# Kernel optimization log

Hardware: AMD Instinct MI355X
Metric: run time of the kernel (lower is better)

Reference implementation:

```python
import jax, jax.numpy as jnp
import numpy as np

N_NODES = 50000
N_EDGES = 640000
DIM_IN = 128
DIM_OUT = 32
NUM_GRAPHS = 64


def setup_inputs() -> dict:
    key = jax.random.key(0)
    ks = jax.random.split(key, 8)
    x = jax.random.normal(ks[0], (N_NODES, DIM_IN), dtype=jnp.float32)
    edge_index = jax.random.randint(ks[1], (2, N_EDGES), 0, N_NODES, dtype=jnp.int64)
    batch = jnp.sort(jax.random.randint(ks[2], (N_NODES,), 0, NUM_GRAPHS, dtype=jnp.int64))
    s = 1.0 / np.sqrt(DIM_IN)
    W1 = jax.random.normal(ks[3], (DIM_IN, DIM_IN), dtype=jnp.float32) * s
    b1 = jnp.zeros((DIM_IN,), dtype=jnp.float32)
    W2 = jax.random.normal(ks[4], (DIM_IN, DIM_IN), dtype=jnp.float32) * s
    b2 = jnp.zeros((DIM_IN,), dtype=jnp.float32)
    Wh = jax.random.normal(ks[5], (DIM_IN, DIM_OUT), dtype=jnp.float32) * s
    bh = jnp.zeros((DIM_OUT,), dtype=jnp.float32)
    return {"x": x, "edge_index": edge_index, "batch": batch,
            "W1": W1, "b1": b1, "W2": W2, "b2": b2, "Wh": Wh, "bh": bh}


def _gcn_conv(x, src, dst, norm, W, b):
    # GCNConv: h = x @ W; out[i] = sum_{(j->i)} norm_e * h[j] + b
    h = x @ W
    msg = h[src] * norm[:, None]                      # [E+N, D] gather + scale
    out = jax.ops.segment_sum(msg, dst, num_segments=x.shape[0])
    return out + b


def reference(x, edge_index, batch, W1, b1, W2, b2, Wh, bh):
    n = x.shape[0]
    loops = jnp.arange(n, dtype=edge_index.dtype)
    src = jnp.concatenate([edge_index[0], loops])     # add self-loops
    dst = jnp.concatenate([edge_index[1], loops])
    # symmetric normalization: deg^{-1/2}[src] * deg^{-1/2}[dst]
    deg = jax.ops.segment_sum(jnp.ones_like(dst, dtype=x.dtype), dst, num_segments=n)
    dinv = jnp.where(deg > 0, jax.lax.rsqrt(deg), 0.0)
    norm = dinv[src] * dinv[dst]

    h = jax.nn.relu(_gcn_conv(x, src, dst, norm, W1, b1))   # dropout = identity (eval)
    h = jax.nn.relu(_gcn_conv(h, src, dst, norm, W2, b2))
    pooled = jax.ops.segment_sum(h, batch, num_segments=NUM_GRAPHS)  # global_add_pool
    logits = pooled @ Wh + bh
    return jax.nn.log_softmax(logits, axis=1)
```

## Files before the change

kernel.cpp:

```cpp
#include <hip/hip_runtime.h>
#include <hip/hip_bf16.h>
#include <math.h>

#define N_NODES 50000
#define N_EDGES 640000
#define DIM     128
#define NGRAPH  64
#define DOUT    32
#define CAP     64
#define LDSS 136
#define LDSF 132

#define G_GEMM  782
#define B_W2    (G_GEMM)
#define N_W2    64
#define B_ZERO  (B_W2 + N_W2)
#define N_ZERO  32
#define B_FILL  (B_ZERO + N_ZERO)
#define N_FILL  2500
#define G_FRONT (B_FILL + N_FILL)

typedef unsigned short u16;
typedef __attribute__((ext_vector_type(8))) short bf16x8;
typedef __attribute__((ext_vector_type(4))) float f32x4;

__device__ __forceinline__ u16 f2bf(float f) {
    unsigned u = __float_as_uint(f);
    return (u16)((u + 0x7FFFu + ((u >> 16) & 1u)) >> 16);
}
__device__ __forceinline__ float bf2f(u16 h) {
    return __uint_as_float(((unsigned)h) << 16);
}
__device__ __forceinline__ short2 cvt2(float x, float y) {
    __hip_bfloat162 h = __float22bfloat162_rn(make_float2(x, y));
    return *(short2*)&h;
}
__device__ __forceinline__ void upk(unsigned u, float& lo, float& hi) {
    lo = __uint_as_float(u << 16);
    hi = __uint_as_float(u & 0xFFFF0000u);
}

__global__ __launch_bounds__(256) void k_front(const float* __restrict__ X,
                                               const int* __restrict__ src,
                                               const int* __restrict__ dst,
                                               int* __restrict__ cnt,
                                               int* __restrict__ bucket,
                                               const float* __restrict__ W1,
                                               const float* __restrict__ W2,
                                               u16* __restrict__ W2s,
                                               float* __restrict__ pooled,
                                               u16* __restrict__ Y) {
    __shared__ u16 Wl[16384];
    int b   = blockIdx.x;
    int tid = threadIdx.x;

    if (b < G_GEMM) {
        const float4* W14 = (const float4*)W1;
#pragma unroll
        for (int i = 0; i < 16; ++i) {
            int q = i * 256 + tid;
            float4 vv = W14[q];
            int base = q * 4;
            int k = base >> 7, n0 = base & 127;
            int rb = ((n0 >> 4) * 4 + (k >> 5)) * 512 + ((k & 31) >> 3) * 128
                   + (k & 7) + (n0 & 15) * 8;
            Wl[rb]      = f2bf(vv.x);
            Wl[rb + 8]  = f2bf(vv.y);
            Wl[rb + 16] = f2bf(vv.z);
            Wl[rb + 24] = f2bf(vv.w);
        }
        int wv   = tid >> 6;
        int lane = tid & 63;
        int row0 = b * 64 + wv * 16;
        int m    = lane & 15;
        int quad = lane >> 4;
        int ar = min(row0 + m, N_NODES - 1);
        const float* Arow = X + (size_t)ar * DIM;
        bf16x8 a[4];
#pragma unroll
        for (int kc = 0; kc < 4; ++kc) {
            const float4* p4 = (const float4*)(Arow + kc * 32 + quad * 8);
            float4 p = p4[0], q = p4[1];
            short2 s0 = cvt2(p.x, p.y), s1 = cvt2(p.z, p.w);
            short2 s2 = cvt2(q.x, q.y), s3 = cvt2(q.z, q.w);
            bf16x8 av;
            av[0] = s0.x; av[1] = s0.y; av[2] = s1.x; av[3] = s1.y;
            av[4] = s2.x; av[5] = s2.y; av[6] = s3.x; av[7] = s3.y;
            a[kc] = av;
        }
        __syncthreads();
#pragma unroll
        for (int nt = 0; nt < 8; ++nt) {
            f32x4 acc = {0.f, 0.f, 0.f, 0.f};
#pragma unroll
            for (int kc = 0; kc < 4; ++kc) {
                bf16x8 bb = *(const bf16x8*)(&Wl[((nt * 4 + kc) * 64 + lane) * 8]);
                acc = __builtin_amdgcn_mfma_f32_16x16x32_bf16(a[kc], bb, acc, 0, 0, 0);
            }
            int col = nt * 16 + m;
#pragma unroll
            for (int r = 0; r < 4; ++r) {
                int rr = row0 + quad * 4 + r;
                if (rr < N_NODES) Y[(size_t)rr * DIM + col] = f2bf(acc[r]);
            }
        }
    } else if (b < B_ZERO) {
        int t = (b - B_W2) * 256 + tid;
        int j = t & 7, lane = (t >> 3) & 63, kc = (t >> 9) & 3, nt = t >> 11;
        int k = kc * 32 + (lane >> 4) * 8 + j;
        int n = nt * 16 + (lane & 15);
        W2s[t] = f2bf(W2[k * 128 + n]);
    } else if (b < B_FILL) {
        int t = (b - B_ZERO) * 256 + tid;
        pooled[t] = 0.f;
    } else {
        int e = (b - B_FILL) * 256 + tid;
        int d = dst[e];
        int s = src[e];
        int pos = atomicAdd(&cnt[d], 1);
        bucket[d * CAP + pos] = s;
    }
}

__global__ __launch_bounds__(256) void k_agg_gemm(const u16* __restrict__ H,
                                                  const int* __restrict__ bucket,
                                                  const int* __restrict__ cnt,
                                                  const float* __restrict__ bias,
                                                  const u16* __restrict__ Ws,
                                                  u16* __restrict__ Y) {
    __shared__ u16 As[16][LDSS];
    int tid    = threadIdx.x;
    int nloc   = tid >> 4;
    int lane16 = tid & 15;
    int node   = blockIdx.x * 16 + nloc;

    int deg = cnt[node];
    float dself = rsqrtf((float)(deg + 1));
    int e0 = node * CAP, e1 = e0 + deg;
    const uint4* H4 = (const uint4*)H;
    uint4 sv = H4[(size_t)node * 16 + lane16];
    float a0[8], a1[8] = {}, a2[8] = {}, a3[8] = {};
    {
        float lo, hi;
        upk(sv.x, lo, hi); a0[0] = dself * lo; a0[1] = dself * hi;
        upk(sv.y, lo, hi); a0[2] = dself * lo; a0[3] = dself * hi;
        upk(sv.z, lo, hi); a0[4] = dself * lo; a0[5] = dself * hi;
        upk(sv.w, lo, hi); a0[6] = dself * lo; a0[7] = dself * hi;
    }
    for (int e = e0; e < e1; e += 8) {
        int4 c0 = *(const int4*)(bucket + e);
        int4 c1 = *(const int4*)(bucket + e + 4);
        int   idx[8];
        float w[8];
        uint4 v[8];
        int   cd[8];
        idx[0] = c0.x; idx[1] = c0.y; idx[2] = c0.z; idx[3] = c0.w;
        idx[4] = c1.x; idx[5] = c1.y; idx[6] = c1.z; idx[7] = c1.w;
#pragma unroll
        for (int u = 0; u < 8; ++u) {
            bool in = (e + u) < e1;
            w[u]   = in ? 1.f : 0.f;
            idx[u] = in ? idx[u] : 0;
        }
#pragma unroll
        for (int u = 0; u < 8; ++u) cd[u] = cnt[idx[u]];
#pragma unroll
        for (int u = 0; u < 8; ++u) v[u] = H4[(size_t)idx[u] * 16 + lane16];
#pragma unroll
        for (int u = 0; u < 8; ++u) w[u] *= rsqrtf((float)(cd[u] + 1));
#pragma unroll
        for (int u = 0; u < 8; ++u) {
            float* a = (u & 3) == 0 ? a0 : (u & 3) == 1 ? a1 : (u & 3) == 2 ? a2 : a3;
            float lo, hi;
            upk(v[u].x, lo, hi); a[0] = fmaf(w[u], lo, a[0]); a[1] = fmaf(w[u], hi, a[1]);
            upk(v[u].y, lo, hi); a[2] = fmaf(w[u], lo, a[2]); a[3] = fmaf(w[u], hi, a[3]);
            upk(v[u].z, lo, hi); a[4] = fmaf(w[u], lo, a[4]); a[5] = fmaf(w[u], hi, a[5]);
            upk(v[u].w, lo, hi); a[6] = fmaf(w[u], lo, a[6]); a[7] = fmaf(w[u], hi, a[7]);
        }
    }
    {
        float di = dself;
        const float4* b4 = (const float4*)bias;
        float4 blo = b4[lane16 * 2], bhi = b4[lane16 * 2 + 1];
        float r0 = fmaxf(di * (a0[0] + a1[0] + a2[0] + a3[0]) + blo.x, 0.f);
        float r1 = fmaxf(di * (a0[1] + a1[1] + a2[1] + a3[1]) + blo.y, 0.f);
        float r2 = fmaxf(di * (a0[2] + a1[2] + a2[2] + a3[2]) + blo.z, 0.f);
        float r3 = fmaxf(di * (a0[3] + a1[3] + a2[3] + a3[3]) + blo.w, 0.f);
        float r4 = fmaxf(di * (a0[4] + a1[4] + a2[4] + a3[4]) + bhi.x, 0.f);
        float r5 = fmaxf(di * (a0[5] + a1[5] + a2[5] + a3[5]) + bhi.y, 0.f);
        float r6 = fmaxf(di * (a0[6] + a1[6] + a2[6] + a3[6]) + bhi.z, 0.f);
        float r7 = fmaxf(di * (a0[7] + a1[7] + a2[7] + a3[7]) + bhi.w, 0.f);
        short2 s0 = cvt2(r0, r1), s1 = cvt2(r2, r3), s2 = cvt2(r4, r5), s3 = cvt2(r6, r7);
        uint4 o;
        o.x = *(unsigned*)&s0; o.y = *(unsigned*)&s1;
        o.z = *(unsigned*)&s2; o.w = *(unsigned*)&s3;
        *(uint4*)(&As[nloc][lane16 * 8]) = o;
    }
    __syncthreads();

    int wv   = tid >> 6;
    int lane = tid & 63;
    int m    = lane & 15;
    int quad = lane >> 4;
    bf16x8 a[4];
#pragma unroll
    for (int kc = 0; kc < 4; ++kc)
        a[kc] = *(const bf16x8*)(&As[m][kc * 32 + quad * 8]);
    float di[4];
#pragma unroll
    for (int r = 0; r < 4; ++r)
        di[r] = rsqrtf((float)(cnt[blockIdx.x * 16 + quad * 4 + r] + 1));
#pragma unroll
    for (int i = 0; i < 2; ++i) {
        int nt = wv * 2 + i;
        f32x4 acc = {0.f, 0.f, 0.f, 0.f};
#pragma unroll
        for (int kc = 0; kc < 4; ++kc) {
            bf16x8 b = *(const bf16x8*)(Ws + ((size_t)(nt * 4 + kc) * 64 + lane) * 8);
            acc = __builtin_amdgcn_mfma_f32_16x16x32_bf16(a[kc], b, acc, 0, 0, 0);
        }
        int col = nt * 16 + m;
#pragma unroll
        for (int r = 0; r < 4; ++r) {
            int rr = blockIdx.x * 16 + quad * 4 + r;
            Y[(size_t)rr * DIM + col] = f2bf(acc[r] * di[r]);
        }
    }
}

__global__ __launch_bounds__(256) void k_agg_pool(const u16* __restrict__ H,
                                                  const int* __restrict__ bucket,
                                                  const int* __restrict__ cnt,
                                                  const float* __restrict__ bias,
                                                  const int* __restrict__ batch,
                                                  float* __restrict__ pooled) {
    __shared__ float As[16][LDSF];
    __shared__ int bs[16];
    int tid  = threadIdx.x;
    int nloc = tid >> 4;
    int lane = tid & 15;
    int node = blockIdx.x * 16 + nloc;

    int deg = cnt[node];
    int e0 = node * CAP, e1 = e0 + deg;
    const uint4* H4 = (const uint4*)H;
    uint4 sv = H4[(size_t)node * 16 + lane];
    float a0[8], a1[8] = {}, a2[8] = {}, a3[8] = {};
    upk(sv.x, a0[0], a0[1]); upk(sv.y, a0[2], a0[3]);
    upk(sv.z, a0[4], a0[5]); upk(sv.w, a0[6], a0[7]);
    for (int e = e0; e < e1; e += 8) {
        int4 c0 = *(const int4*)(bucket + e);
        int4 c1 = *(const int4*)(bucket + e + 4);
        int   idx[8];
        float w[8];
        uint4 v[8];
        idx[0] = c0.x; idx[1] = c0.y; idx[2] = c0.z; idx[3] = c0.w;
        idx[4] = c1.x; idx[5] = c1.y; idx[6] = c1.z; idx[7] = c1.w;
#pragma unroll
        for (int u = 0; u < 8; ++u) {
            bool in = (e + u) < e1;
            w[u]   = in ? 1.f : 0.f;
            idx[u] = in ? idx[u] : 0;
        }
#pragma unroll
        for (int u = 0; u < 8; ++u) v[u] = H4[(size_t)idx[u] * 16 + lane];
#pragma unroll
        for (int u = 0; u < 8; ++u) {
            float* a = (u & 3) == 0 ? a0 : (u & 3) == 1 ? a1 : (u & 3) == 2 ? a2 : a3;
            float lo, hi;
            upk(v[u].x, lo, hi); a[0] = fmaf(w[u], lo, a[0]); a[1] = fmaf(w[u], hi, a[1]);
            upk(v[u].y, lo, hi); a[2] = fmaf(w[u], lo, a[2]); a[3] = fmaf(w[u], hi, a[3]);
            upk(v[u].z, lo, hi); a[4] = fmaf(w[u], lo, a[4]); a[5] = fmaf(w[u], hi, a[5]);
            upk(v[u].w, lo, hi); a[6] = fmaf(w[u], lo, a[6]); a[7] = fmaf(w[u], hi, a[7]);
        }
    }
    {
        float di = rsqrtf((float)(deg + 1));
        const float4* b4 = (const float4*)bias;
        float4 blo = b4[lane * 2], bhi = b4[lane * 2 + 1];
        float4 olo, ohi;
        olo.x = fmaxf(di * (a0[0] + a1[0] + a2[0] + a3[0]) + blo.x, 0.f);
        olo.y = fmaxf(di * (a0[1] + a1[1] + a2[1] + a3[1]) + blo.y, 0.f);
        olo.z = fmaxf(di * (a0[2] + a1[2] + a2[2] + a3[2]) + blo.z, 0.f);
        olo.w = fmaxf(di * (a0[3] + a1[3] + a2[3] + a3[3]) + blo.w, 0.f);
        ohi.x = fmaxf(di * (a0[4] + a1[4] + a2[4] + a3[4]) + bhi.x, 0.f);
        ohi.y = fmaxf(di * (a0[5] + a1[5] + a2[5] + a3[5]) + bhi.y, 0.f);
        ohi.z = fmaxf(di * (a0[6] + a1[6] + a2[6] + a3[6]) + bhi.z, 0.f);
        ohi.w = fmaxf(di * (a0[7] + a1[7] + a2[7] + a3[7]) + bhi.w, 0.f);
        *(float4*)(&As[nloc][lane * 8])     = olo;
        *(float4*)(&As[nloc][lane * 8 + 4]) = ohi;
    }
    if (lane == 0) bs[nloc] = batch[node];
    __syncthreads();

    if (tid < 128) {
        float acc = 0.f;
        int cb = bs[0];
#pragma unroll
        for (int n = 0; n < 16; ++n) {
            int b = bs[n];
            if (b != cb) {
                atomicAdd(&pooled[cb * DIM + tid], acc);
                acc = 0.f; cb = b;
            }
            acc += As[n][tid];
        }
        atomicAdd(&pooled[cb * DIM + tid], acc);
    }
}

__global__ __launch_bounds__(64) void k_head(const float* __restrict__ pooled,
                                             const float* __restrict__ Wh,
                                             const float* __restrict__ bh,
                                             float* __restrict__ out) {
    int g = blockIdx.x;
    int lane = threadIdx.x;
    int c = lane & 31;
    const float* p = pooled + g * DIM;
    float lg = bh[c];
#pragma unroll 8
    for (int k = 0; k < DIM; ++k) lg = fmaf(p[k], Wh[k * DOUT + c], lg);
    float m = lg;
    for (int off = 16; off >= 1; off >>= 1) m = fmaxf(m, __shfl_xor(m, off, 32));
    float ex = expf(lg - m);
    float s = ex;
    for (int off = 16; off >= 1; off >>= 1) s += __shfl_xor(s, off, 32);
    if (lane < 32) out[g * DOUT + c] = lg - m - logf(s);
}

extern "C" void kernel_launch(void* const* d_in, const int* in_sizes, int n_in,
                              void* d_out, int out_size, void* d_ws, size_t ws_size,
                              hipStream_t stream) {
    const float* x     = (const float*)d_in[0];
    const int*   ei    = (const int*)d_in[1];
    const int*   batch = (const int*)d_in[2];
    const float* W1    = (const float*)d_in[3];
    const float* b1    = (const float*)d_in[4];
    const float* W2    = (const float*)d_in[5];
    const float* b2    = (const float*)d_in[6];
    const float* Wh    = (const float*)d_in[7];
    const float* bh    = (const float*)d_in[8];
    float* out = (float*)d_out;
    const int* src = ei;
    const int* dst = ei + N_EDGES;

    char* ws = (char*)d_ws;
    size_t off = 0;
    auto alloc = [&](size_t bytes) {
        void* p = ws + off;
        off += (bytes + 255) & ~(size_t)255;
        return p;
    };
    u16*   bufA   = (u16*) alloc((size_t)N_NODES * DIM * 2);
    u16*   bufB   = (u16*) alloc((size_t)N_NODES * DIM * 2);
    int*   cnt    = (int*) alloc((size_t)N_NODES * 4);
    int*   bucket = (int*) alloc((size_t)N_NODES * CAP * 4);
    u16*   W2s    = (u16*) alloc((size_t)DIM * DIM * 2);
    float* pooled = (float*)alloc((size_t)NGRAPH * DIM * 4);
    (void)ws_size; (void)in_sizes; (void)n_in; (void)out_size;

    hipMemsetAsync(cnt, 0, (size_t)N_NODES * 4, stream);

    k_front   <<<G_FRONT, 256, 0, stream>>>(x, src, dst, cnt, bucket, W1, W2,
                                            W2s, pooled, bufA);
    k_agg_gemm<<<N_NODES / 16, 256, 0, stream>>>(bufA, bucket, cnt, b1, W2s, bufB);
    k_agg_pool<<<N_NODES / 16, 256, 0, stream>>>(bufB, bucket, cnt, b2, batch, pooled);

    k_head<<<NGRAPH, 64, 0, stream>>>(pooled, Wh, bh, out);
}
```

Before: 197.0 us.

## Pre-swizzle W1 in a prep kernel and prefetch bucket indices in aggregation

Moves the bf16 conversion and swizzle of W1 (plus the W2 swizzle and the pooled zeroing) into a small separate prep kernel. The GEMM blocks in k_front now read pre-swizzled W1 fragments straight from global memory instead of each of the 782 blocks rebuilding a 32KB LDS copy and waiting on a barrier. Dropping the LDS allocation frees occupancy in the front kernel. The aggregation kernels also software-prefetch the next 8 bucket indices one iteration ahead, at the cost of an extra kernel launch and some register pressure.

```diff
diff --git a/kernel.cpp b/kernel.cpp
--- a/kernel.cpp
+++ b/kernel.cpp
@@ -12,13 +12,8 @@
 #define LDSF 132
 
 #define G_GEMM  782
-#define B_W2    (G_GEMM)
-#define N_W2    64
-#define B_ZERO  (B_W2 + N_W2)
-#define N_ZERO  32
-#define B_FILL  (B_ZERO + N_ZERO)
 #define N_FILL  2500
-#define G_FRONT (B_FILL + N_FILL)
+#define G_FRONT (G_GEMM + N_FILL)
 
 typedef unsigned short u16;
 typedef __attribute__((ext_vector_type(8))) short bf16x8;
@@ -38,6 +33,26 @@
 __device__ __forceinline__ void upk(unsigned u, float& lo, float& hi) {
     lo = __uint_as_float(u << 16);
     hi = __uint_as_float(u & 0xFFFF0000u);
+}
+
+__global__ __launch_bounds__(256) void k_prep(const float* __restrict__ W1,
+                                              const float* __restrict__ W2,
+                                              u16* __restrict__ W1s,
+                                              u16* __restrict__ W2s,
+                                              float* __restrict__ pooled) {
+    int b = blockIdx.x;
+    int tid = threadIdx.x;
+    if (b < 128) {
+        int t = (b & 63) * 256 + tid;
+        int j = t & 7, lane = (t >> 3) & 63, kc = (t >> 9) & 3, nt = t >> 11;
+        int k = kc * 32 + (lane >> 4) * 8 + j;
+        int n = nt * 16 + (lane & 15);
+        if (b < 64) W1s[t] = f2bf(W1[k * 128 + n]);
+        else        W2s[t] = f2bf(W2[k * 128 + n]);
+    } else {
+        int t = (b - 128) * 256 + tid;
+        pooled[t] = 0.f;
+    }
 }
 
 __global__ __launch_bounds__(256) void k_front(const float* __restrict__ X,
@@ -45,30 +60,12 @@
                                                const int* __restrict__ dst,
                                                int* __restrict__ cnt,
                                                int* __restrict__ bucket,
-                                               const float* __restrict__ W1,
-                                               const float* __restrict__ W2,
-                                               u16* __restrict__ W2s,
-                                               float* __restrict__ pooled,
+                                               const u16* __restrict__ Ws,
                                                u16* __restrict__ Y) {
-    __shared__ u16 Wl[16384];
     int b   = blockIdx.x;
     int tid = threadIdx.x;
 
     if (b < G_GEMM) {
-        const float4* W14 = (const float4*)W1;
-#pragma unroll
-        for (int i = 0; i < 16; ++i) {
-            int q = i * 256 + tid;
-            float4 vv = W14[q];
-            int base = q * 4;
-            int k = base >> 7, n0 = base & 127;
-            int rb = ((n0 >> 4) * 4 + (k >> 5)) * 512 + ((k & 31) >> 3) * 128
-                   + (k & 7) + (n0 & 15) * 8;
-            Wl[rb]      = f2bf(vv.x);
-            Wl[rb + 8]  = f2bf(vv.y);
-            Wl[rb + 16] = f2bf(vv.z);
-            Wl[rb + 24] = f2bf(vv.w);
-        }
         int wv   = tid >> 6;
         int lane = tid & 63;
         int row0 = b * 64 + wv * 16;
@@ -88,13 +85,12 @@
             av[4] = s2.x; av[5] = s2.y; av[6] = s3.x; av[7] = s3.y;
             a[kc] = av;
         }
-        __syncthreads();
 #pragma unroll
         for (int nt = 0; nt < 8; ++nt) {
             f32x4 acc = {0.f, 0.f, 0.f, 0.f};
 #pragma unroll
             for (int kc = 0; kc < 4; ++kc) {
-                bf16x8 bb = *(const bf16x8*)(&Wl[((nt * 4 + kc) * 64 + lane) * 8]);
+                bf16x8 bb = *(const bf16x8*)(Ws + ((size_t)(nt * 4 + kc) * 64 + lane) * 8);
                 acc = __builtin_amdgcn_mfma_f32_16x16x32_bf16(a[kc], bb, acc, 0, 0, 0);
             }
             int col = nt * 16 + m;
@@ -104,19 +100,10 @@
                 if (rr < N_NODES) Y[(size_t)rr * DIM + col] = f2bf(acc[r]);
             }
         }
-    } else if (b < B_ZERO) {
-        int t = (b - B_W2) * 256 + tid;
-        int j = t & 7, lane = (t >> 3) & 63, kc = (t >> 9) & 3, nt = t >> 11;
-        int k = kc * 32 + (lane >> 4) * 8 + j;
-        int n = nt * 16 + (lane & 15);
-        W2s[t] = f2bf(W2[k * 128 + n]);
-    } else if (b < B_FILL) {
-        int t = (b - B_ZERO) * 256 + tid;
-        pooled[t] = 0.f;
     } else {
-        int e = (b - B_FILL) * 256 + tid;
+        int e = (b - G_GEMM) * 256 + tid;
+        int s = src[e];
         int d = dst[e];
-        int s = src[e];
         int pos = atomicAdd(&cnt[d], 1);
         bucket[d * CAP + pos] = s;
     }
@@ -147,15 +134,20 @@
         upk(sv.z, lo, hi); a0[4] = dself * lo; a0[5] = dself * hi;
         upk(sv.w, lo, hi); a0[6] = dself * lo; a0[7] = dself * hi;
     }
+    int4 c0, c1;
+    if (e0 < e1) { c0 = *(const int4*)(bucket + e0); c1 = *(const int4*)(bucket + e0 + 4); }
     for (int e = e0; e < e1; e += 8) {
-        int4 c0 = *(const int4*)(bucket + e);
-        int4 c1 = *(const int4*)(bucket + e + 4);
+        int4 p0 = c0, p1 = c1;
+        if (e + 8 < e1) {
+            c0 = *(const int4*)(bucket + e + 8);
+            c1 = *(const int4*)(bucket + e + 12);
+        }
         int   idx[8];
         float w[8];
         uint4 v[8];
         int   cd[8];
-        idx[0] = c0.x; idx[1] = c0.y; idx[2] = c0.z; idx[3] = c0.w;
-        idx[4] = c1.x; idx[5] = c1.y; idx[6] = c1.z; idx[7] = c1.w;
+        idx[0] = p0.x; idx[1] = p0.y; idx[2] = p0.z; idx[3] = p0.w;
+        idx[4] = p1.x; idx[5] = p1.y; idx[6] = p1.z; idx[7] = p1.w;
 #pragma unroll
         for (int u = 0; u < 8; ++u) {
             bool in = (e + u) < e1;
@@ -248,14 +240,19 @@
     float a0[8], a1[8] = {}, a2[8] = {}, a3[8] = {};
     upk(sv.x, a0[0], a0[1]); upk(sv.y, a0[2], a0[3]);
     upk(sv.z, a0[4], a0[5]); upk(sv.w, a0[6], a0[7]);
+    int4 c0, c1;
+    if (e0 < e1) { c0 = *(const int4*)(bucket + e0); c1 = *(const int4*)(bucket + e0 + 4); }
     for (int e = e0; e < e1; e += 8) {
-        int4 c0 = *(const int4*)(bucket + e);
-        int4 c1 = *(const int4*)(bucket + e + 4);
+        int4 p0 = c0, p1 = c1;
+        if (e + 8 < e1) {
+            c0 = *(const int4*)(bucket + e + 8);
+            c1 = *(const int4*)(bucket + e + 12);
+        }
         int   idx[8];
         float w[8];
         uint4 v[8];
-        idx[0] = c0.x; idx[1] = c0.y; idx[2] = c0.z; idx[3] = c0.w;
-        idx[4] = c1.x; idx[5] = c1.y; idx[6] = c1.z; idx[7] = c1.w;
+        idx[0] = p0.x; idx[1] = p0.y; idx[2] = p0.z; idx[3] = p0.w;
+        idx[4] = p1.x; idx[5] = p1.y; idx[6] = p1.z; idx[7] = p1.w;
 #pragma unroll
         for (int u = 0; u < 8; ++u) {
             bool in = (e + u) < e1;
@@ -355,14 +352,15 @@
     u16*   bufB   = (u16*) alloc((size_t)N_NODES * DIM * 2);
     int*   cnt    = (int*) alloc((size_t)N_NODES * 4);
     int*   bucket = (int*) alloc((size_t)N_NODES * CAP * 4);
+    u16*   W1s    = (u16*) alloc((size_t)DIM * DIM * 2);
     u16*   W2s    = (u16*) alloc((size_t)DIM * DIM * 2);
     float* pooled = (float*)alloc((size_t)NGRAPH * DIM * 4);
     (void)ws_size; (void)in_sizes; (void)n_in; (void)out_size;
 
     hipMemsetAsync(cnt, 0, (size_t)N_NODES * 4, stream);
 
-    k_front   <<<G_FRONT, 256, 0, stream>>>(x, src, dst, cnt, bucket, W1, W2,
-                                            W2s, pooled, bufA);
+    k_prep    <<<160, 256, 0, stream>>>(W1, W2, W1s, W2s, pooled);
+    k_front   <<<G_FRONT, 256, 0, stream>>>(x, src, dst, cnt, bucket, W1s, bufA);
     k_agg_gemm<<<N_NODES / 16, 256, 0, stream>>>(bufA, bucket, cnt, b1, W2s, bufB);
     k_agg_pool<<<N_NODES / 16, 256, 0, stream>>>(bufB, bucket, cnt, b2, batch, pooled);
 
```

After: 192.8 us. 2.1% less time.
